# Kernel optimization log

Hardware: AMD Instinct MI355X
Metric: run time of the kernel (lower is better)

Reference implementation:

```python
import jax, jax.numpy as jnp
import numpy as np

N_NODES = 50000
N_EDGES = 150000
D = 512
N_LAYERS = 4
BN_EPS = 1e-5


def setup_inputs() -> dict:
    key = jax.random.key(0)
    ks = jax.random.split(key, 8)
    scale = 1.0 / np.sqrt(D)
    x = jax.random.normal(ks[0], (N_NODES, D), dtype=jnp.float32)
    W1 = jax.random.normal(ks[1], (N_LAYERS, D, D), dtype=jnp.float32) * scale
    b1 = jax.random.normal(ks[2], (N_LAYERS, D), dtype=jnp.float32) * 0.01
    gamma = jnp.ones((N_LAYERS, D), dtype=jnp.float32)
    beta = jnp.zeros((N_LAYERS, D), dtype=jnp.float32)
    W2 = jax.random.normal(ks[3], (N_LAYERS, D, D), dtype=jnp.float32) * scale
    b2 = jax.random.normal(ks[4], (N_LAYERS, D), dtype=jnp.float32) * 0.01
    src = jax.random.randint(ks[5], (N_EDGES,), 0, N_NODES, dtype=jnp.int32)
    dst = jax.random.randint(ks[6], (N_EDGES,), 0, N_NODES, dtype=jnp.int32)
    return {"x": x, "W1": W1, "b1": b1, "gamma": gamma, "beta": beta,
            "W2": W2, "b2": b2, "src": src, "dst": dst}


def _gin_layer(h, src, dst, W1, b1, gamma, beta, W2, b2):
    # GIN sum aggregation: agg[v] = sum_{(u->v) in E} h[u]; eps = 0
    agg = jax.ops.segment_sum(h[src], dst, num_segments=N_NODES)
    z = jnp.dot(h + agg, W1.T) + b1                      # [N, D] Linear1
    # BatchNorm1d (training mode: batch stats, biased variance)
    mu = jnp.mean(z, axis=0)
    var = jnp.mean(jnp.square(z - mu), axis=0)
    z = (z - mu) * jax.lax.rsqrt(var + BN_EPS) * gamma + beta
    z = jax.nn.relu(z)
    return jnp.dot(z, W2.T) + b2                          # [N, D] Linear2


def reference(x, W1, b1, gamma, beta, W2, b2, src, dst):
    h = x
    outs = []
    for i in range(N_LAYERS):
        h = _gin_layer(h, src, dst, W1[i], b1[i], gamma[i], beta[i], W2[i], b2[i])
        outs.append(h)
    # single graph: dgl.mean_nodes == mean over all nodes, squeeze -> [D]
    return (jnp.mean(outs[-1], axis=0), jnp.mean(outs[-2], axis=0))
```

## Files before the change

kernel.cpp:

```cpp
#include <hip/hip_runtime.h>

#define NN 50000
#define MPAD 50176
#define DD 512
#define NE 150000

typedef float f32x2 __attribute__((ext_vector_type(2)));
typedef float f32x4 __attribute__((ext_vector_type(4)));
typedef float f32x8 __attribute__((ext_vector_type(8)));
typedef __bf16 bf16x8 __attribute__((ext_vector_type(8)));
typedef unsigned short u16x8 __attribute__((ext_vector_type(8)));
typedef unsigned int u32x2 __attribute__((ext_vector_type(2)));

__device__ __forceinline__ void gload16(const void* g, void* l) {
  __builtin_amdgcn_global_load_lds((const __attribute__((address_space(1))) void*)g,
                                   (__attribute__((address_space(3))) void*)l, 16, 0, 0);
}

__device__ __forceinline__ u32x2 f32x8_to_fp8(f32x8 v) {
  int t0 = __builtin_amdgcn_cvt_pk_fp8_f32(v[0], v[1], 0, false);
  t0 = __builtin_amdgcn_cvt_pk_fp8_f32(v[2], v[3], t0, true);
  int t1 = __builtin_amdgcn_cvt_pk_fp8_f32(v[4], v[5], 0, false);
  t1 = __builtin_amdgcn_cvt_pk_fp8_f32(v[6], v[7], t1, true);
  u32x2 r;
  r[0] = (unsigned)t0;
  r[1] = (unsigned)t1;
  return r;
}
__device__ __forceinline__ f32x8 fp8x8_to_f32(u32x2 u) {
  f32x2 a = __builtin_amdgcn_cvt_pk_f32_fp8((int)u[0], false);
  f32x2 b = __builtin_amdgcn_cvt_pk_f32_fp8((int)u[0], true);
  f32x2 c = __builtin_amdgcn_cvt_pk_f32_fp8((int)u[1], false);
  f32x2 d = __builtin_amdgcn_cvt_pk_f32_fp8((int)u[1], true);
  f32x8 v;
  v[0]=a[0]; v[1]=a[1]; v[2]=b[0]; v[3]=b[1]; v[4]=c[0]; v[5]=c[1]; v[6]=d[0]; v[7]=d[1];
  return v;
}

#define READ_FRAGS(la, lb, kk, AV, BV)                                                       \
  {                                                                                          \
    const int so = (((kk) * 4 + fg) ^ sx) * 8;                                               \
    _Pragma("unroll") for (int i = 0; i < 4; ++i)                                            \
        AV[i] = *reinterpret_cast<const bf16x8*>(&(la)[(rg + i * 16 + fr) * 64 + so]);       \
    _Pragma("unroll") for (int j = 0; j < 4; ++j)                                            \
        BV[j] = *reinterpret_cast<const bf16x8*>(&(lb)[(cg + j * 16 + fr) * 64 + so]);       \
  }

#define MFMA16(AV, BV)                                                                       \
  _Pragma("unroll") for (int i = 0; i < 4; ++i)                                              \
      _Pragma("unroll") for (int j = 0; j < 4; ++j)                                          \
          acc[i][j] = __builtin_amdgcn_mfma_f32_16x16x32_bf16(AV[i], BV[j], acc[i][j], 0, 0, 0);

#define PHASE_TAIL(AV, BV)                                                                   \
  __builtin_amdgcn_s_barrier();                                                              \
  asm volatile("s_waitcnt lgkmcnt(0)" ::: "memory");                                         \
  __builtin_amdgcn_sched_barrier(0);                                                         \
  __builtin_amdgcn_s_setprio(1);                                                             \
  MFMA16(AV, BV);                                                                            \
  __builtin_amdgcn_s_setprio(0);

__global__ void wconv0_k(const float* __restrict__ W1, unsigned short* __restrict__ o1) {
  const size_t i = ((size_t)blockIdx.x * 256 + threadIdx.x) * 8;
  const f32x4* g = reinterpret_cast<const f32x4*>(W1 + i);
  f32x4 a = g[0], b = g[1];
  f32x8 v;
  v[0]=a[0]; v[1]=a[1]; v[2]=a[2]; v[3]=a[3]; v[4]=b[0]; v[5]=b[1]; v[6]=b[2]; v[7]=b[3];
  *reinterpret_cast<bf16x8*>(o1 + i) = __builtin_convertvector(v, bf16x8);
}

__global__ __launch_bounds__(256) void trans_k(const float* __restrict__ W2,
                                               float* __restrict__ W2T) {
  __shared__ float t[64][65];
  const int l = blockIdx.z;
  const int a0 = blockIdx.x * 64;
  const int b0 = blockIdx.y * 64;
  const float* src = W2 + (size_t)l * DD * DD;
  float* dst = W2T + (size_t)l * DD * DD;
#pragma unroll
  for (int q = 0; q < 16; ++q) {
    const int idx = q * 256 + threadIdx.x;
    const int r = idx >> 6, c = idx & 63;
    t[r][c] = src[(size_t)(a0 + r) * DD + b0 + c];
  }
  __syncthreads();
#pragma unroll
  for (int q = 0; q < 16; ++q) {
    const int idx = q * 256 + threadIdx.x;
    const int r = idx >> 6, c = idx & 63;
    dst[(size_t)(b0 + r) * DD + a0 + c] = t[c][r];
  }
}

__global__ __launch_bounds__(256) void wfuse_k(const float* __restrict__ W1all,
                                               const float* __restrict__ W2T,
                                               unsigned short* __restrict__ WF) {
  constexpr int LDK = 72;
  __shared__ unsigned short lA[128 * LDK];
  __shared__ unsigned short lB[128 * LDK];
  const int l = blockIdx.z;
  const float* A = W1all + (size_t)(l + 1) * DD * DD;
  const float* Bt = W2T + (size_t)l * DD * DD;
  unsigned short* out = WF + (size_t)l * DD * DD;
  const int tid = threadIdx.x;
  const int brow = blockIdx.y * 128;
  const int bcol = blockIdx.x * 128;
  const int lane = tid & 63;
  const int w = tid >> 6;
  const int wr = (w >> 1) * 64;
  const int wc = (w & 1) * 64;
  const int fr = lane & 15;
  const int fg = lane >> 4;
  f32x4 acc[4][4] = {};
  const int srow = tid >> 3;
  const int scol = (tid & 7) * 8;
  for (int kt = 0; kt < 8; ++kt) {
    const int k0 = kt * 64 + scol;
    __syncthreads();
#pragma unroll
    for (int p = 0; p < 4; ++p) {
      const int r = srow + 32 * p;
      {
        const f32x4* g = reinterpret_cast<const f32x4*>(A + (size_t)(brow + r) * DD + k0);
        f32x4 v0 = g[0], v1 = g[1];
        f32x8 vf;
        vf[0]=v0[0]; vf[1]=v0[1]; vf[2]=v0[2]; vf[3]=v0[3];
        vf[4]=v1[0]; vf[5]=v1[1]; vf[6]=v1[2]; vf[7]=v1[3];
        *reinterpret_cast<bf16x8*>(&lA[r * LDK + scol]) = __builtin_convertvector(vf, bf16x8);
      }
      {
        const f32x4* g = reinterpret_cast<const f32x4*>(Bt + (size_t)(bcol + r) * DD + k0);
        f32x4 v0 = g[0], v1 = g[1];
        f32x8 vf;
        vf[0]=v0[0]; vf[1]=v0[1]; vf[2]=v0[2]; vf[3]=v0[3];
        vf[4]=v1[0]; vf[5]=v1[1]; vf[6]=v1[2]; vf[7]=v1[3];
        *reinterpret_cast<bf16x8*>(&lB[r * LDK + scol]) = __builtin_convertvector(vf, bf16x8);
      }
    }
    __syncthreads();
#pragma unroll
    for (int kk = 0; kk < 2; ++kk) {
      bf16x8 av[4], bv[4];
#pragma unroll
      for (int i = 0; i < 4; ++i)
        av[i] = *reinterpret_cast<const bf16x8*>(&lA[(wr + i * 16 + fr) * LDK + kk * 32 + fg * 8]);
#pragma unroll
      for (int j = 0; j < 4; ++j)
        bv[j] = *reinterpret_cast<const bf16x8*>(&lB[(wc + j * 16 + fr) * LDK + kk * 32 + fg * 8]);
#pragma unroll
      for (int i = 0; i < 4; ++i)
#pragma unroll
        for (int j = 0; j < 4; ++j)
          acc[i][j] = __builtin_amdgcn_mfma_f32_16x16x32_bf16(av[i], bv[j], acc[i][j], 0, 0, 0);
    }
  }
#pragma unroll
  for (int j = 0; j < 4; ++j) {
    const int col = bcol + wc + j * 16 + fr;
#pragma unroll
    for (int i = 0; i < 4; ++i) {
      const int rb = brow + wr + i * 16 + fg * 4;
#pragma unroll
      for (int r = 0; r < 4; ++r) {
        __bf16 b = (__bf16)acc[i][j][r];
        out[(size_t)(rb + r) * DD + col] = __builtin_bit_cast(unsigned short, b);
      }
    }
  }
}

__global__ __launch_bounds__(512) void cvec_k(const float* __restrict__ W1all,
                                              const float* __restrict__ b2all,
                                              float* __restrict__ cvec) {
  __shared__ float bb[DD];
  const int l = blockIdx.x;
  bb[threadIdx.x] = b2all[(size_t)l * DD + threadIdx.x];
  __syncthreads();
  const float* row = W1all + (size_t)(l + 1) * DD * DD + (size_t)threadIdx.x * DD;
  float s = 0.f;
  for (int a = 0; a < DD; a += 4) {
    f32x4 v = *reinterpret_cast<const f32x4*>(row + a);
    s += v[0] * bb[a] + v[1] * bb[a + 1] + v[2] * bb[a + 2] + v[3] * bb[a + 3];
  }
  cvec[l * DD + threadIdx.x] = s;
}

__global__ void count_k(const int* __restrict__ dst, int* __restrict__ cnt) {
  const int e = blockIdx.x * 256 + threadIdx.x;
  if (e < NE) atomicAdd(&cnt[dst[e]], 1);
}

__global__ __launch_bounds__(1024) void scan_k(const int* __restrict__ cnt,
                                               int* __restrict__ rowptr,
                                               int* __restrict__ cursor) {
  __shared__ int wsum[16];
  __shared__ int base_s;
  if (threadIdx.x == 0) base_s = 0;
  __syncthreads();
  const int lane = threadIdx.x & 63;
  const int wid = threadIdx.x >> 6;
  for (int c0 = 0; c0 < NN; c0 += 1024) {
    const int i = c0 + threadIdx.x;
    const int v = (i < NN) ? cnt[i] : 0;
    int incl = v;
#pragma unroll
    for (int d = 1; d < 64; d <<= 1) {
      int t = __shfl_up(incl, d);
      if (lane >= d) incl += t;
    }
    if (lane == 63) wsum[wid] = incl;
    __syncthreads();
    if (wid == 0 && lane < 16) {
      int wv = wsum[lane];
#pragma unroll
      for (int d = 1; d < 16; d <<= 1) {
        int t = __shfl_up(wv, d);
        if (lane >= d) wv += t;
      }
      wsum[lane] = wv;
    }
    __syncthreads();
    const int waveoff = wid ? wsum[wid - 1] : 0;
    const int excl = base_s + waveoff + incl - v;
    if (i < NN) {
      rowptr[i] = excl;
      cursor[i] = excl;
    }
    __syncthreads();
    if (threadIdx.x == 0) base_s += wsum[15];
    __syncthreads();
  }
  if (threadIdx.x == 0) rowptr[NN] = base_s;
}

__global__ void fill_k(const int* __restrict__ src, const int* __restrict__ dst,
                       int* __restrict__ cursor, int* __restrict__ csrc) {
  const int e = blockIdx.x * 256 + threadIdx.x;
  if (e < NE) {
    const int pos = atomicAdd(&cursor[dst[e]], 1);
    csrc[pos] = src[e];
  }
}

__global__ void degp1_k(const int* __restrict__ rowptr, float* __restrict__ degp1) {
  const int i = blockIdx.x * 256 + threadIdx.x;
  if (i < MPAD) degp1[i] = (i < NN) ? (float)(1 + rowptr[i + 1] - rowptr[i]) : 0.f;
}

__global__ __launch_bounds__(256) void agg_f32_k(const float* __restrict__ h,
                                                 const int* __restrict__ rowptr,
                                                 const int* __restrict__ csrc,
                                                 unsigned short* __restrict__ xout) {
  const int node = blockIdx.x * 4 + (threadIdx.x >> 6);
  const int lane = threadIdx.x & 63;
  const f32x4* row = reinterpret_cast<const f32x4*>(h + (size_t)node * DD + lane * 8);
  f32x4 a0 = row[0], a1 = row[1];
  f32x4 b0 = {}, b1 = {};
  const int p1 = rowptr[node + 1];
  int p = rowptr[node];
  for (; p + 1 < p1; p += 2) {
    const int s0 = csrc[p];
    const int s1 = csrc[p + 1];
    const f32x4* r0 = reinterpret_cast<const f32x4*>(h + (size_t)s0 * DD + lane * 8);
    const f32x4* r1 = reinterpret_cast<const f32x4*>(h + (size_t)s1 * DD + lane * 8);
    a0 += r0[0]; a1 += r0[1];
    b0 += r1[0]; b1 += r1[1];
  }
  if (p < p1) {
    const int s0 = csrc[p];
    const f32x4* r0 = reinterpret_cast<const f32x4*>(h + (size_t)s0 * DD + lane * 8);
    a0 += r0[0]; a1 += r0[1];
  }
  a0 += b0; a1 += b1;
  f32x8 vf;
  vf[0]=a0[0]; vf[1]=a0[1]; vf[2]=a0[2]; vf[3]=a0[3];
  vf[4]=a1[0]; vf[5]=a1[1]; vf[6]=a1[2]; vf[7]=a1[3];
  *reinterpret_cast<bf16x8*>(xout + (size_t)node * DD + lane * 8) =
      __builtin_convertvector(vf, bf16x8);
}

__global__ __launch_bounds__(256) void agg_act_k(const unsigned char* __restrict__ z,
                                                 const float* __restrict__ scsh,
                                                 const int* __restrict__ rowptr,
                                                 const int* __restrict__ csrc,
                                                 unsigned short* __restrict__ xout) {
  const int node = blockIdx.x * 4 + (threadIdx.x >> 6);
  const int lane = threadIdx.x & 63;
  const int c0 = lane * 8;
  f32x4 sca = *reinterpret_cast<const f32x4*>(scsh + c0);
  f32x4 scb = *reinterpret_cast<const f32x4*>(scsh + c0 + 4);
  f32x4 sha = *reinterpret_cast<const f32x4*>(scsh + DD + c0);
  f32x4 shb = *reinterpret_cast<const f32x4*>(scsh + DD + c0 + 4);
#define ACT8(dst, uv)                                                    \
  {                                                                      \
    f32x8 f_ = fp8x8_to_f32(uv);                                         \
    _Pragma("unroll") for (int q = 0; q < 4; ++q) {                      \
      dst[q]     += fmaxf(f_[q]     * sca[q] + sha[q], 0.f);             \
      dst[q + 4] += fmaxf(f_[q + 4] * scb[q] + shb[q], 0.f);             \
    }                                                                    \
  }
  f32x8 acc = {}, acc2 = {};
  u32x2 sv = *reinterpret_cast<const u32x2*>(z + (size_t)node * DD + c0);
  ACT8(acc, sv)
  const int p1 = rowptr[node + 1];
  int p = rowptr[node];
  for (; p + 1 < p1; p += 2) {
    const int s0 = csrc[p];
    const int s1 = csrc[p + 1];
    u32x2 r0 = *reinterpret_cast<const u32x2*>(z + (size_t)s0 * DD + c0);
    u32x2 r1 = *reinterpret_cast<const u32x2*>(z + (size_t)s1 * DD + c0);
    ACT8(acc, r0)
    ACT8(acc2, r1)
  }
  if (p < p1) {
    const int s0 = csrc[p];
    u32x2 r0 = *reinterpret_cast<const u32x2*>(z + (size_t)s0 * DD + c0);
    ACT8(acc, r0)
  }
  acc += acc2;
#undef ACT8
  *reinterpret_cast<bf16x8*>(xout + (size_t)node * DD + c0) =
      __builtin_convertvector(acc, bf16x8);
}

__global__ __launch_bounds__(256) void colsum_act_k(const unsigned char* __restrict__ z,
                                                    const float* __restrict__ scsh,
                                                    float* __restrict__ cs) {
  __shared__ float red[4][DD];
  const int g = threadIdx.x >> 6;
  const int lane = threadIdx.x & 63;
  const int c0 = lane * 8;
  f32x4 sca = *reinterpret_cast<const f32x4*>(scsh + c0);
  f32x4 scb = *reinterpret_cast<const f32x4*>(scsh + c0 + 4);
  f32x4 sha = *reinterpret_cast<const f32x4*>(scsh + DD + c0);
  f32x4 shb = *reinterpret_cast<const f32x4*>(scsh + DD + c0 + 4);
  f32x8 acc = {};
  for (int rr = g; rr < 128; rr += 4) {
    const int row = blockIdx.x * 128 + rr;
    if (row < NN) {
      u32x2 rv = *reinterpret_cast<const u32x2*>(z + (size_t)row * DD + c0);
      f32x8 f = fp8x8_to_f32(rv);
#pragma unroll
      for (int q = 0; q < 4; ++q) {
        acc[q]     += fmaxf(f[q]     * sca[q] + sha[q], 0.f);
        acc[q + 4] += fmaxf(f[q + 4] * scb[q] + shb[q], 0.f);
      }
    }
  }
#pragma unroll
  for (int q = 0; q < 8; ++q) red[g][c0 + q] = acc[q];
  __syncthreads();
  for (int cc = threadIdx.x; cc < DD; cc += 256) {
    const float s = red[0][cc] + red[1][cc] + red[2][cc] + red[3][cc];
    atomicAdd(&cs[cc], s);
  }
}

__global__ void bnfin_k(float* __restrict__ stats, const float* __restrict__ gamma,
                        const float* __restrict__ beta, float* __restrict__ scsh) {
  const int n = threadIdx.x;
  const float inv = 1.0f / (float)NN;
  const float mu = stats[n] * inv;
  const float var = stats[DD + n] * inv - mu * mu;
  const float sc = rsqrtf(var + 1e-5f) * gamma[n];
  scsh[n] = sc;
  scsh[DD + n] = beta[n] - mu * sc;
  stats[n] = 0.f;
  stats[DD + n] = 0.f;
}

__global__ __launch_bounds__(512, 2) void gemmf_k(
    const unsigned short* __restrict__ A, const unsigned short* __restrict__ B,
    unsigned char* __restrict__ Z, float* __restrict__ stats,
    const float* __restrict__ degp1, const float* __restrict__ cvec) {
  __shared__ unsigned short sm[73728];
  constexpr int AOFF[3] = {0, 16384, 8192};
  constexpr int BOFF[3] = {24576, 57344, 40960};
  const int tid = threadIdx.x;
  const int lane = tid & 63;
  const int w = tid >> 6;
  const int rg = (w >> 2) * 64;
  const int cg = (w & 3) * 64;
  const int fr = lane & 15;
  const int fg = lane >> 4;
  const int sx = fr & 7;
  const int bid = blockIdx.x;
  const int swb = (bid & 7) * 98 + (bid >> 3);
  const int brow = (swb >> 1) * 128;
  const int bcol = (swb & 1) * 256;
  const char* Ab = (const char*)A + (size_t)brow * 1024;
  const char* Bb = (const char*)B + (size_t)bcol * 1024;
  const int srow = tid >> 3;
  const int sce = (tid & 7) * 8;
  const int sswz = (((tid & 7) ^ (srow & 7))) * 16;

  f32x4 acc[4][4] = {};

#pragma unroll
  for (int t = 0; t < 2; ++t) {
#pragma unroll
    for (int i = 0; i < 2; ++i)
      gload16(Ab + (size_t)(i * 64 + srow) * 1024 + t * 128 + sswz,
              &sm[AOFF[t] + (i * 64 + srow) * 64 + sce]);
#pragma unroll
    for (int i = 0; i < 4; ++i)
      gload16(Bb + (size_t)(i * 64 + srow) * 1024 + t * 128 + sswz,
              &sm[BOFF[t] + (i * 64 + srow) * 64 + sce]);
  }

#pragma unroll
  for (int kt = 0; kt < 8; ++kt) {
    if (kt < 7) asm volatile("s_waitcnt vmcnt(6)" ::: "memory");
    else        asm volatile("s_waitcnt vmcnt(0)" ::: "memory");
    __builtin_amdgcn_s_barrier();
    const unsigned short* la = &sm[AOFF[kt % 3]];
    const unsigned short* lb = &sm[BOFF[kt % 3]];
    bf16x8 av[4], bv[4];
    READ_FRAGS(la, lb, 0, av, bv);
    if (kt + 2 < 8) {
      const int t2 = kt + 2;
#pragma unroll
      for (int i = 0; i < 2; ++i)
        gload16(Ab + (size_t)(i * 64 + srow) * 1024 + t2 * 128 + sswz,
                &sm[AOFF[t2 % 3] + (i * 64 + srow) * 64 + sce]);
      gload16(Bb + (size_t)srow * 1024 + t2 * 128 + sswz,
              &sm[BOFF[t2 % 3] + srow * 64 + sce]);
    }
    PHASE_TAIL(av, bv)
    __builtin_amdgcn_s_barrier();
    READ_FRAGS(la, lb, 1, av, bv);
    if (kt + 2 < 8) {
      const int t2 = kt + 2;
#pragma unroll
      for (int i = 1; i < 4; ++i)
        gload16(Bb + (size_t)(i * 64 + srow) * 1024 + t2 * 128 + sswz,
                &sm[BOFF[t2 % 3] + (i * 64 + srow) * 64 + sce]);
    }
    PHASE_TAIL(av, bv)
  }

  if (cvec != nullptr) {
    float cj[4];
#pragma unroll
    for (int j = 0; j < 4; ++j) cj[j] = cvec[bcol + cg + j * 16 + fr];
#pragma unroll
    for (int i = 0; i < 4; ++i)
#pragma unroll
      for (int r = 0; r < 4; ++r) {
        const float dgv = degp1[brow + rg + i * 16 + fg * 4 + r];
#pragma unroll
        for (int j = 0; j < 4; ++j) acc[i][j][r] += dgv * cj[j];
      }
  }

#pragma unroll
  for (int j = 0; j < 4; ++j) {
    const int col = bcol + cg + j * 16 + fr;
    float s1 = 0.f, s2 = 0.f;
#pragma unroll
    for (int i = 0; i < 4; ++i)
#pragma unroll
      for (int r = 0; r < 4; ++r) {
        const float v = acc[i][j][r];
        s1 += v;
        s2 += v * v;
      }
    s1 += __shfl_down(s1, 32);
    s2 += __shfl_down(s2, 32);
    s1 += __shfl_down(s1, 16);
    s2 += __shfl_down(s2, 16);
    if (lane < 16) {
      atomicAdd(&stats[col], s1);
      atomicAdd(&stats[DD + col], s2);
    }
  }

  unsigned short* C = &sm[24576];
#pragma unroll
  for (int j = 0; j < 4; ++j)
#pragma unroll
    for (int i = 0; i < 4; ++i)
#pragma unroll
      for (int r = 0; r < 4; ++r) {
        const int row = rg + i * 16 + fg * 4 + r;
        const int col = cg + j * 16 + fr;
        __bf16 b = (__bf16)acc[i][j][r];
        C[row * 256 + (((col >> 3) ^ (row & 7)) << 3) + (col & 7)] =
            __builtin_bit_cast(unsigned short, b);
      }
  asm volatile("s_waitcnt lgkmcnt(0)" ::: "memory");
  __builtin_amdgcn_s_barrier();
  const int orow = tid >> 2;
  const int ox = orow & 7;
  const unsigned short* cr = &C[orow * 256];
  unsigned char* zg = Z + (size_t)(brow + orow) * DD + bcol;
#pragma unroll
  for (int i = 0; i < 8; ++i) {
    const int s = (tid & 3) * 8 + ((i + tid) & 7);
    u16x8 cv = *reinterpret_cast<const u16x8*>(cr + (s ^ ox) * 8);
    f32x8 cf = __builtin_convertvector(__builtin_bit_cast(bf16x8, cv), f32x8);
    *reinterpret_cast<u32x2*>(zg + s * 8) = f32x8_to_fp8(cf);
  }
}

__global__ __launch_bounds__(256) void out_k(const float* __restrict__ cs3,
                                             const float* __restrict__ cs2,
                                             const float* __restrict__ W2all,
                                             const float* __restrict__ b2all,
                                             float* __restrict__ out) {
  const int o = blockIdx.x * 4 + (threadIdx.x >> 6);
  const int lane = threadIdx.x & 63;
  const int layer = (o < DD) ? 3 : 2;
  const int n = o & (DD - 1);
  const float* cs = (o < DD) ? cs3 : cs2;
  const float* row = W2all + (size_t)layer * DD * DD + (size_t)n * DD + lane * 8;
  f32x4 w0 = *reinterpret_cast<const f32x4*>(row);
  f32x4 w1 = *reinterpret_cast<const f32x4*>(row + 4);
  f32x4 c0 = *reinterpret_cast<const f32x4*>(cs + lane * 8);
  f32x4 c1 = *reinterpret_cast<const f32x4*>(cs + lane * 8 + 4);
  float s = w0[0]*c0[0] + w0[1]*c0[1] + w0[2]*c0[2] + w0[3]*c0[3]
          + w1[0]*c1[0] + w1[1]*c1[1] + w1[2]*c1[2] + w1[3]*c1[3];
#pragma unroll
  for (int d = 32; d > 0; d >>= 1) s += __shfl_down(s, d);
  if (lane == 0) out[o] = s / (float)NN + b2all[layer * DD + n];
}

extern "C" void kernel_launch(void* const* d_in, const int* in_sizes, int n_in,
                              void* d_out, int out_size, void* d_ws, size_t ws_size,
                              hipStream_t stream) {
  const float* x     = (const float*)d_in[0];
  const float* W1    = (const float*)d_in[1];
  const float* gamma = (const float*)d_in[3];
  const float* beta  = (const float*)d_in[4];
  const float* W2    = (const float*)d_in[5];
  const float* b2    = (const float*)d_in[6];
  const int*   src   = (const int*)d_in[7];
  const int*   dst   = (const int*)d_in[8];
  float* out = (float*)d_out;

  char* ws = (char*)d_ws;
  const size_t ABYTES = (size_t)MPAD * DD * 2;
  const size_t ZBYTES = (size_t)MPAD * DD;
  unsigned short* xact   = (unsigned short*)(ws);
  unsigned char*  z      = (unsigned char*)(ws + ABYTES);
  unsigned short* wb1    = (unsigned short*)(ws + ABYTES + ZBYTES);
  unsigned short* wf     = (unsigned short*)(ws + ABYTES + ZBYTES + 524288);
  float*          w2t    = (float*)(ws + ABYTES + ZBYTES + 2097152);
  float*          cvec   = (float*)(ws + ABYTES + ZBYTES + 5242880);
  float*          cs2    = (float*)(ws + ABYTES + ZBYTES + 5251072);
  float*          cs3    = (float*)(ws + ABYTES + ZBYTES + 5255168);
  float*          stats  = (float*)(ws + ABYTES + ZBYTES + 5259264);
  float*          scsh   = (float*)(ws + ABYTES + ZBYTES + 5263360);
  float*          degp1  = (float*)(ws + ABYTES + ZBYTES + 5267456);
  int*            rowptr = (int*)(ws + ABYTES + ZBYTES + 5468160);
  int*            cursor = (int*)(ws + ABYTES + ZBYTES + 5668864);
  int*            csrc   = (int*)(ws + ABYTES + ZBYTES + 5869568);

  wconv0_k<<<128, 256, 0, stream>>>(W1, wb1);
  trans_k<<<dim3(8, 8, 3), 256, 0, stream>>>(W2, w2t);
  wfuse_k<<<dim3(4, 4, 3), 256, 0, stream>>>(W1, w2t, wf);
  cvec_k<<<3, 512, 0, stream>>>(W1, b2, cvec);

  hipMemsetAsync(xact + (size_t)NN * DD, 0, (size_t)(MPAD - NN) * DD * 2, stream);
  hipMemsetAsync(cs2, 0, DD * sizeof(float), stream);
  hipMemsetAsync(cs3, 0, DD * sizeof(float), stream);
  hipMemsetAsync(stats, 0, 2 * DD * sizeof(float), stream);

  hipMemsetAsync(cursor, 0, NN * sizeof(int), stream);
  count_k<<<(NE + 255) / 256, 256, 0, stream>>>(dst, cursor);
  scan_k<<<1, 1024, 0, stream>>>(cursor, rowptr, cursor);
  fill_k<<<(NE + 255) / 256, 256, 0, stream>>>(src, dst, cursor, csrc);
  degp1_k<<<(MPAD + 255) / 256, 256, 0, stream>>>(rowptr, degp1);

  agg_f32_k<<<NN / 4, 256, 0, stream>>>(x, rowptr, csrc, xact);
  gemmf_k<<<784, 512, 0, stream>>>(xact, wb1, z, stats, degp1, nullptr);
  bnfin_k<<<1, DD, 0, stream>>>(stats, gamma, beta, scsh);

  for (int l = 0; l < 3; ++l) {
    agg_act_k<<<NN / 4, 256, 0, stream>>>(z, scsh, rowptr, csrc, xact);
    if (l == 2) colsum_act_k<<<392, 256, 0, stream>>>(z, scsh, cs2);
    gemmf_k<<<784, 512, 0, stream>>>(xact, wf + (size_t)l * DD * DD, z, stats,
                                     degp1, cvec + l * DD);
    bnfin_k<<<1, DD, 0, stream>>>(stats, gamma + (l + 1) * DD, beta + (l + 1) * DD, scsh);
  }

  colsum_act_k<<<392, 256, 0, stream>>>(z, scsh, cs3);
  out_k<<<256, 256, 0, stream>>>(cs3, cs2, W2, b2, out);
}
```

Baseline: 580.9 us.

## Fuse preprocessing kernels into three multi-role launches and gather fp8 input

```diff
diff --git a/kernel.cpp b/kernel.cpp
--- a/kernel.cpp
+++ b/kernel.cpp
@@ -59,134 +59,42 @@
   MFMA16(AV, BV);                                                                            \
   __builtin_amdgcn_s_setprio(0);
 
-__global__ void wconv0_k(const float* __restrict__ W1, unsigned short* __restrict__ o1) {
-  const size_t i = ((size_t)blockIdx.x * 256 + threadIdx.x) * 8;
-  const f32x4* g = reinterpret_cast<const f32x4*>(W1 + i);
-  f32x4 a = g[0], b = g[1];
-  f32x8 v;
-  v[0]=a[0]; v[1]=a[1]; v[2]=a[2]; v[3]=a[3]; v[4]=b[0]; v[5]=b[1]; v[6]=b[2]; v[7]=b[3];
-  *reinterpret_cast<bf16x8*>(o1 + i) = __builtin_convertvector(v, bf16x8);
-}
-
-__global__ __launch_bounds__(256) void trans_k(const float* __restrict__ W2,
-                                               float* __restrict__ W2T) {
-  __shared__ float t[64][65];
-  const int l = blockIdx.z;
-  const int a0 = blockIdx.x * 64;
-  const int b0 = blockIdx.y * 64;
-  const float* src = W2 + (size_t)l * DD * DD;
-  float* dst = W2T + (size_t)l * DD * DD;
-#pragma unroll
-  for (int q = 0; q < 16; ++q) {
-    const int idx = q * 256 + threadIdx.x;
-    const int r = idx >> 6, c = idx & 63;
-    t[r][c] = src[(size_t)(a0 + r) * DD + b0 + c];
-  }
-  __syncthreads();
-#pragma unroll
-  for (int q = 0; q < 16; ++q) {
-    const int idx = q * 256 + threadIdx.x;
-    const int r = idx >> 6, c = idx & 63;
-    dst[(size_t)(b0 + r) * DD + a0 + c] = t[c][r];
-  }
-}
-
-__global__ __launch_bounds__(256) void wfuse_k(const float* __restrict__ W1all,
-                                               const float* __restrict__ W2T,
-                                               unsigned short* __restrict__ WF) {
-  constexpr int LDK = 72;
-  __shared__ unsigned short lA[128 * LDK];
-  __shared__ unsigned short lB[128 * LDK];
-  const int l = blockIdx.z;
-  const float* A = W1all + (size_t)(l + 1) * DD * DD;
-  const float* Bt = W2T + (size_t)l * DD * DD;
-  unsigned short* out = WF + (size_t)l * DD * DD;
+__global__ __launch_bounds__(256) void prep1_k(
+    const float* __restrict__ x, const float* __restrict__ W1,
+    const int* __restrict__ dst, unsigned char* __restrict__ xq,
+    unsigned short* __restrict__ wb1, int* __restrict__ cnt,
+    unsigned short* __restrict__ xact, float* __restrict__ stats,
+    float* __restrict__ cs2, float* __restrict__ cs3) {
+  const int b = blockIdx.x;
   const int tid = threadIdx.x;
-  const int brow = blockIdx.y * 128;
-  const int bcol = blockIdx.x * 128;
-  const int lane = tid & 63;
-  const int w = tid >> 6;
-  const int wr = (w >> 1) * 64;
-  const int wc = (w & 1) * 64;
-  const int fr = lane & 15;
-  const int fg = lane >> 4;
-  f32x4 acc[4][4] = {};
-  const int srow = tid >> 3;
-  const int scol = (tid & 7) * 8;
-  for (int kt = 0; kt < 8; ++kt) {
-    const int k0 = kt * 64 + scol;
-    __syncthreads();
-#pragma unroll
-    for (int p = 0; p < 4; ++p) {
-      const int r = srow + 32 * p;
-      {
-        const f32x4* g = reinterpret_cast<const f32x4*>(A + (size_t)(brow + r) * DD + k0);
-        f32x4 v0 = g[0], v1 = g[1];
-        f32x8 vf;
-        vf[0]=v0[0]; vf[1]=v0[1]; vf[2]=v0[2]; vf[3]=v0[3];
-        vf[4]=v1[0]; vf[5]=v1[1]; vf[6]=v1[2]; vf[7]=v1[3];
-        *reinterpret_cast<bf16x8*>(&lA[r * LDK + scol]) = __builtin_convertvector(vf, bf16x8);
-      }
-      {
-        const f32x4* g = reinterpret_cast<const f32x4*>(Bt + (size_t)(bcol + r) * DD + k0);
-        f32x4 v0 = g[0], v1 = g[1];
-        f32x8 vf;
-        vf[0]=v0[0]; vf[1]=v0[1]; vf[2]=v0[2]; vf[3]=v0[3];
-        vf[4]=v1[0]; vf[5]=v1[1]; vf[6]=v1[2]; vf[7]=v1[3];
-        *reinterpret_cast<bf16x8*>(&lB[r * LDK + scol]) = __builtin_convertvector(vf, bf16x8);
-      }
-    }
-    __syncthreads();
-#pragma unroll
-    for (int kk = 0; kk < 2; ++kk) {
-      bf16x8 av[4], bv[4];
-#pragma unroll
-      for (int i = 0; i < 4; ++i)
-        av[i] = *reinterpret_cast<const bf16x8*>(&lA[(wr + i * 16 + fr) * LDK + kk * 32 + fg * 8]);
-#pragma unroll
-      for (int j = 0; j < 4; ++j)
-        bv[j] = *reinterpret_cast<const bf16x8*>(&lB[(wc + j * 16 + fr) * LDK + kk * 32 + fg * 8]);
-#pragma unroll
-      for (int i = 0; i < 4; ++i)
-#pragma unroll
-        for (int j = 0; j < 4; ++j)
-          acc[i][j] = __builtin_amdgcn_mfma_f32_16x16x32_bf16(av[i], bv[j], acc[i][j], 0, 0, 0);
-    }
-  }
-#pragma unroll
-  for (int j = 0; j < 4; ++j) {
-    const int col = bcol + wc + j * 16 + fr;
-#pragma unroll
-    for (int i = 0; i < 4; ++i) {
-      const int rb = brow + wr + i * 16 + fg * 4;
-#pragma unroll
-      for (int r = 0; r < 4; ++r) {
-        __bf16 b = (__bf16)acc[i][j][r];
-        out[(size_t)(rb + r) * DD + col] = __builtin_bit_cast(unsigned short, b);
-      }
-    }
-  }
-}
-
-__global__ __launch_bounds__(512) void cvec_k(const float* __restrict__ W1all,
-                                              const float* __restrict__ b2all,
-                                              float* __restrict__ cvec) {
-  __shared__ float bb[DD];
-  const int l = blockIdx.x;
-  bb[threadIdx.x] = b2all[(size_t)l * DD + threadIdx.x];
-  __syncthreads();
-  const float* row = W1all + (size_t)(l + 1) * DD * DD + (size_t)threadIdx.x * DD;
-  float s = 0.f;
-  for (int a = 0; a < DD; a += 4) {
-    f32x4 v = *reinterpret_cast<const f32x4*>(row + a);
-    s += v[0] * bb[a] + v[1] * bb[a + 1] + v[2] * bb[a + 2] + v[3] * bb[a + 3];
-  }
-  cvec[l * DD + threadIdx.x] = s;
-}
-
-__global__ void count_k(const int* __restrict__ dst, int* __restrict__ cnt) {
-  const int e = blockIdx.x * 256 + threadIdx.x;
-  if (e < NE) atomicAdd(&cnt[dst[e]], 1);
+  if (b < 12500) {
+    const size_t i = ((size_t)b * 256 + tid) * 8;
+    const f32x4* g = reinterpret_cast<const f32x4*>(x + i);
+    f32x4 a = g[0], c = g[1];
+    f32x8 v;
+    v[0]=a[0]; v[1]=a[1]; v[2]=a[2]; v[3]=a[3]; v[4]=c[0]; v[5]=c[1]; v[6]=c[2]; v[7]=c[3];
+    *reinterpret_cast<u32x2*>(xq + i) = f32x8_to_fp8(v);
+  } else if (b < 12628) {
+    const size_t i = ((size_t)(b - 12500) * 256 + tid) * 8;
+    const f32x4* g = reinterpret_cast<const f32x4*>(W1 + i);
+    f32x4 a = g[0], c = g[1];
+    f32x8 v;
+    v[0]=a[0]; v[1]=a[1]; v[2]=a[2]; v[3]=a[3]; v[4]=c[0]; v[5]=c[1]; v[6]=c[2]; v[7]=c[3];
+    *reinterpret_cast<bf16x8*>(wb1 + i) = __builtin_convertvector(v, bf16x8);
+  } else if (b < 13214) {
+    const int e = (b - 12628) * 256 + tid;
+    if (e < NE) atomicAdd(&cnt[dst[e]], 1);
+  } else if (b < 13258) {
+    const int i = (b - 13214) * 256 + tid;
+    u16x8 zz = {};
+    *reinterpret_cast<u16x8*>(xact + (size_t)NN * DD + (size_t)i * 8) = zz;
+  } else {
+    for (int i = tid; i < 2 * DD; i += 256) stats[i] = 0.f;
+    for (int i = tid; i < DD; i += 256) {
+      cs2[i] = 0.f;
+      cs3[i] = 0.f;
+    }
+  }
 }
 
 __global__ __launch_bounds__(1024) void scan_k(const int* __restrict__ cnt,
@@ -232,50 +140,173 @@
   if (threadIdx.x == 0) rowptr[NN] = base_s;
 }
 
-__global__ void fill_k(const int* __restrict__ src, const int* __restrict__ dst,
-                       int* __restrict__ cursor, int* __restrict__ csrc) {
-  const int e = blockIdx.x * 256 + threadIdx.x;
-  if (e < NE) {
-    const int pos = atomicAdd(&cursor[dst[e]], 1);
-    csrc[pos] = src[e];
-  }
-}
-
-__global__ void degp1_k(const int* __restrict__ rowptr, float* __restrict__ degp1) {
-  const int i = blockIdx.x * 256 + threadIdx.x;
-  if (i < MPAD) degp1[i] = (i < NN) ? (float)(1 + rowptr[i + 1] - rowptr[i]) : 0.f;
-}
-
-__global__ __launch_bounds__(256) void agg_f32_k(const float* __restrict__ h,
-                                                 const int* __restrict__ rowptr,
-                                                 const int* __restrict__ csrc,
-                                                 unsigned short* __restrict__ xout) {
+__global__ __launch_bounds__(256) void prep2_k(
+    const int* __restrict__ src, const int* __restrict__ dst,
+    int* __restrict__ cursor, int* __restrict__ csrc,
+    const float* __restrict__ W2, float* __restrict__ W2T) {
+  __shared__ float t[64][65];
+  const int b = blockIdx.x;
+  const int tid = threadIdx.x;
+  if (b < 586) {
+    const int e = b * 256 + tid;
+    if (e < NE) {
+      const int pos = atomicAdd(&cursor[dst[e]], 1);
+      csrc[pos] = src[e];
+    }
+  } else {
+    const int q = b - 586;
+    const int l = q >> 6;
+    const int rem = q & 63;
+    const int a0 = (rem >> 3) * 64;
+    const int b0 = (rem & 7) * 64;
+    const float* sp = W2 + (size_t)l * DD * DD;
+    float* dp = W2T + (size_t)l * DD * DD;
+#pragma unroll
+    for (int k = 0; k < 16; ++k) {
+      const int idx = k * 256 + tid;
+      const int r = idx >> 6, c = idx & 63;
+      t[r][c] = sp[(size_t)(a0 + r) * DD + b0 + c];
+    }
+    __syncthreads();
+#pragma unroll
+    for (int k = 0; k < 16; ++k) {
+      const int idx = k * 256 + tid;
+      const int r = idx >> 6, c = idx & 63;
+      dp[(size_t)(b0 + r) * DD + a0 + c] = t[c][r];
+    }
+  }
+}
+
+__global__ __launch_bounds__(256) void prep3_k(
+    const float* __restrict__ W1all, const float* __restrict__ W2T,
+    unsigned short* __restrict__ WF, const float* __restrict__ b2all,
+    float* __restrict__ cvec, const int* __restrict__ rowptr,
+    float* __restrict__ degp1) {
+  __shared__ char pl[36864];
+  const int b = blockIdx.x;
+  const int tid = threadIdx.x;
+  if (b < 48) {
+    constexpr int LDK = 72;
+    unsigned short* lA = (unsigned short*)pl;
+    unsigned short* lB = (unsigned short*)(pl + 18432);
+    const int l = b >> 4;
+    const int rem = b & 15;
+    const int brow = (rem >> 2) * 128;
+    const int bcol = (rem & 3) * 128;
+    const float* A = W1all + (size_t)(l + 1) * DD * DD;
+    const float* Bt = W2T + (size_t)l * DD * DD;
+    unsigned short* out = WF + (size_t)l * DD * DD;
+    const int lane = tid & 63;
+    const int w = tid >> 6;
+    const int wr = (w >> 1) * 64;
+    const int wc = (w & 1) * 64;
+    const int fr = lane & 15;
+    const int fg = lane >> 4;
+    f32x4 acc[4][4] = {};
+    const int srow = tid >> 3;
+    const int scol = (tid & 7) * 8;
+    for (int kt = 0; kt < 8; ++kt) {
+      const int k0 = kt * 64 + scol;
+      __syncthreads();
+#pragma unroll
+      for (int p = 0; p < 4; ++p) {
+        const int r = srow + 32 * p;
+        {
+          const f32x4* g = reinterpret_cast<const f32x4*>(A + (size_t)(brow + r) * DD + k0);
+          f32x4 v0 = g[0], v1 = g[1];
+          f32x8 vf;
+          vf[0]=v0[0]; vf[1]=v0[1]; vf[2]=v0[2]; vf[3]=v0[3];
+          vf[4]=v1[0]; vf[5]=v1[1]; vf[6]=v1[2]; vf[7]=v1[3];
+          *reinterpret_cast<bf16x8*>(&lA[r * LDK + scol]) = __builtin_convertvector(vf, bf16x8);
+        }
+        {
+          const f32x4* g = reinterpret_cast<const f32x4*>(Bt + (size_t)(bcol + r) * DD + k0);
+          f32x4 v0 = g[0], v1 = g[1];
+          f32x8 vf;
+          vf[0]=v0[0]; vf[1]=v0[1]; vf[2]=v0[2]; vf[3]=v0[3];
+          vf[4]=v1[0]; vf[5]=v1[1]; vf[6]=v1[2]; vf[7]=v1[3];
+          *reinterpret_cast<bf16x8*>(&lB[r * LDK + scol]) = __builtin_convertvector(vf, bf16x8);
+        }
+      }
+      __syncthreads();
+#pragma unroll
+      for (int kk = 0; kk < 2; ++kk) {
+        bf16x8 av[4], bv[4];
+#pragma unroll
+        for (int i = 0; i < 4; ++i)
+          av[i] = *reinterpret_cast<const bf16x8*>(&lA[(wr + i * 16 + fr) * LDK + kk * 32 + fg * 8]);
+#pragma unroll
+        for (int j = 0; j < 4; ++j)
+          bv[j] = *reinterpret_cast<const bf16x8*>(&lB[(wc + j * 16 + fr) * LDK + kk * 32 + fg * 8]);
+#pragma unroll
+        for (int i = 0; i < 4; ++i)
+#pragma unroll
+          for (int j = 0; j < 4; ++j)
+            acc[i][j] = __builtin_amdgcn_mfma_f32_16x16x32_bf16(av[i], bv[j], acc[i][j], 0, 0, 0);
+      }
+    }
+#pragma unroll
+    for (int j = 0; j < 4; ++j) {
+      const int col = bcol + wc + j * 16 + fr;
+#pragma unroll
+      for (int i = 0; i < 4; ++i) {
+        const int rb = brow + wr + i * 16 + fg * 4;
+#pragma unroll
+        for (int r = 0; r < 4; ++r) {
+          __bf16 bb = (__bf16)acc[i][j][r];
+          out[(size_t)(rb + r) * DD + col] = __builtin_bit_cast(unsigned short, bb);
+        }
+      }
+    }
+  } else if (b < 51) {
+    const int l = b - 48;
+    float* bb = (float*)pl;
+    bb[tid] = b2all[(size_t)l * DD + tid];
+    bb[tid + 256] = b2all[(size_t)l * DD + tid + 256];
+    __syncthreads();
+#pragma unroll
+    for (int rep = 0; rep < 2; ++rep) {
+      const int n = tid + rep * 256;
+      const float* row = W1all + (size_t)(l + 1) * DD * DD + (size_t)n * DD;
+      float s = 0.f;
+      for (int a = 0; a < DD; a += 4) {
+        f32x4 v = *reinterpret_cast<const f32x4*>(row + a);
+        s += v[0] * bb[a] + v[1] * bb[a + 1] + v[2] * bb[a + 2] + v[3] * bb[a + 3];
+      }
+      cvec[l * DD + n] = s;
+    }
+  } else {
+    const int i = (b - 51) * 256 + tid;
+    if (i < MPAD) degp1[i] = (i < NN) ? (float)(1 + rowptr[i + 1] - rowptr[i]) : 0.f;
+  }
+}
+
+__global__ __launch_bounds__(256) void agg_x_k(const unsigned char* __restrict__ xq,
+                                               const int* __restrict__ rowptr,
+                                               const int* __restrict__ csrc,
+                                               unsigned short* __restrict__ xout) {
   const int node = blockIdx.x * 4 + (threadIdx.x >> 6);
   const int lane = threadIdx.x & 63;
-  const f32x4* row = reinterpret_cast<const f32x4*>(h + (size_t)node * DD + lane * 8);
-  f32x4 a0 = row[0], a1 = row[1];
-  f32x4 b0 = {}, b1 = {};
+  const int c0 = lane * 8;
+  f32x8 acc = fp8x8_to_f32(*reinterpret_cast<const u32x2*>(xq + (size_t)node * DD + c0));
+  f32x8 acc2 = {};
   const int p1 = rowptr[node + 1];
   int p = rowptr[node];
   for (; p + 1 < p1; p += 2) {
     const int s0 = csrc[p];
     const int s1 = csrc[p + 1];
-    const f32x4* r0 = reinterpret_cast<const f32x4*>(h + (size_t)s0 * DD + lane * 8);
-    const f32x4* r1 = reinterpret_cast<const f32x4*>(h + (size_t)s1 * DD + lane * 8);
-    a0 += r0[0]; a1 += r0[1];
-    b0 += r1[0]; b1 += r1[1];
+    u32x2 r0 = *reinterpret_cast<const u32x2*>(xq + (size_t)s0 * DD + c0);
+    u32x2 r1 = *reinterpret_cast<const u32x2*>(xq + (size_t)s1 * DD + c0);
+    acc += fp8x8_to_f32(r0);
+    acc2 += fp8x8_to_f32(r1);
   }
   if (p < p1) {
     const int s0 = csrc[p];
-    const f32x4* r0 = reinterpret_cast<const f32x4*>(h + (size_t)s0 * DD + lane * 8);
-    a0 += r0[0]; a1 += r0[1];
-  }
-  a0 += b0; a1 += b1;
-  f32x8 vf;
-  vf[0]=a0[0]; vf[1]=a0[1]; vf[2]=a0[2]; vf[3]=a0[3];
-  vf[4]=a1[0]; vf[5]=a1[1]; vf[6]=a1[2]; vf[7]=a1[3];
-  *reinterpret_cast<bf16x8*>(xout + (size_t)node * DD + lane * 8) =
-      __builtin_convertvector(vf, bf16x8);
+    acc += fp8x8_to_f32(*reinterpret_cast<const u32x2*>(xq + (size_t)s0 * DD + c0));
+  }
+  acc += acc2;
+  *reinterpret_cast<bf16x8*>(xout + (size_t)node * DD + c0) =
+      __builtin_convertvector(acc, bf16x8);
 }
 
 __global__ __launch_bounds__(256) void agg_act_k(const unsigned char* __restrict__ z,
@@ -538,40 +569,29 @@
   float* out = (float*)d_out;
 
   char* ws = (char*)d_ws;
-  const size_t ABYTES = (size_t)MPAD * DD * 2;
-  const size_t ZBYTES = (size_t)MPAD * DD;
   unsigned short* xact   = (unsigned short*)(ws);
-  unsigned char*  z      = (unsigned char*)(ws + ABYTES);
-  unsigned short* wb1    = (unsigned short*)(ws + ABYTES + ZBYTES);
-  unsigned short* wf     = (unsigned short*)(ws + ABYTES + ZBYTES + 524288);
-  float*          w2t    = (float*)(ws + ABYTES + ZBYTES + 2097152);
-  float*          cvec   = (float*)(ws + ABYTES + ZBYTES + 5242880);
-  float*          cs2    = (float*)(ws + ABYTES + ZBYTES + 5251072);
-  float*          cs3    = (float*)(ws + ABYTES + ZBYTES + 5255168);
-  float*          stats  = (float*)(ws + ABYTES + ZBYTES + 5259264);
-  float*          scsh   = (float*)(ws + ABYTES + ZBYTES + 5263360);
-  float*          degp1  = (float*)(ws + ABYTES + ZBYTES + 5267456);
-  int*            rowptr = (int*)(ws + ABYTES + ZBYTES + 5468160);
-  int*            cursor = (int*)(ws + ABYTES + ZBYTES + 5668864);
-  int*            csrc   = (int*)(ws + ABYTES + ZBYTES + 5869568);
-
-  wconv0_k<<<128, 256, 0, stream>>>(W1, wb1);
-  trans_k<<<dim3(8, 8, 3), 256, 0, stream>>>(W2, w2t);
-  wfuse_k<<<dim3(4, 4, 3), 256, 0, stream>>>(W1, w2t, wf);
-  cvec_k<<<3, 512, 0, stream>>>(W1, b2, cvec);
-
-  hipMemsetAsync(xact + (size_t)NN * DD, 0, (size_t)(MPAD - NN) * DD * 2, stream);
-  hipMemsetAsync(cs2, 0, DD * sizeof(float), stream);
-  hipMemsetAsync(cs3, 0, DD * sizeof(float), stream);
-  hipMemsetAsync(stats, 0, 2 * DD * sizeof(float), stream);
+  unsigned char*  z      = (unsigned char*)(ws + 51380224);
+  unsigned char*  xq     = (unsigned char*)(ws + 77070336);
+  unsigned short* wb1    = (unsigned short*)(ws + 102670336);
+  unsigned short* wf     = (unsigned short*)(ws + 103194624);
+  float*          w2t    = (float*)(ws + 104767488);
+  float*          cvec   = (float*)(ws + 107913216);
+  float*          cs2    = (float*)(ws + 107921408);
+  float*          cs3    = (float*)(ws + 107923456);
+  float*          stats  = (float*)(ws + 107925504);
+  float*          scsh   = (float*)(ws + 107929600);
+  float*          degp1  = (float*)(ws + 107933696);
+  int*            rowptr = (int*)(ws + 108134400);
+  int*            cursor = (int*)(ws + 108334592);
+  int*            csrc   = (int*)(ws + 108534784);
 
   hipMemsetAsync(cursor, 0, NN * sizeof(int), stream);
-  count_k<<<(NE + 255) / 256, 256, 0, stream>>>(dst, cursor);
+  prep1_k<<<13259, 256, 0, stream>>>(x, W1, dst, xq, wb1, cursor, xact, stats, cs2, cs3);
   scan_k<<<1, 1024, 0, stream>>>(cursor, rowptr, cursor);
-  fill_k<<<(NE + 255) / 256, 256, 0, stream>>>(src, dst, cursor, csrc);
-  degp1_k<<<(MPAD + 255) / 256, 256, 0, stream>>>(rowptr, degp1);
-
-  agg_f32_k<<<NN / 4, 256, 0, stream>>>(x, rowptr, csrc, xact);
+  prep2_k<<<778, 256, 0, stream>>>(src, dst, cursor, csrc, W2, w2t);
+  prep3_k<<<247, 256, 0, stream>>>(W1, w2t, wf, b2, cvec, rowptr, degp1);
+
+  agg_x_k<<<NN / 4, 256, 0, stream>>>(xq, rowptr, csrc, xact);
   gemmf_k<<<784, 512, 0, stream>>>(xact, wb1, z, stats, degp1, nullptr);
   bnfin_k<<<1, DD, 0, stream>>>(stats, gamma, beta, scsh);
 
```

Measured after the change: 530.6 us. 8.7% less time.
